# Optimization experiments

Measured on AMD Instinct MI355X. Metric: run time of the kernel, lower is better.

The kernel has to match this reference:

```python
import jax, jax.numpy as jnp
import numpy as np

N = 32                      # rotation matrix size (n x n)
INPUT_DIM = 512
HIDDEN = 1024
BATCH = 16384
NUM_ANGLES = N * (N - 1) // 2   # 496

# Givens plane indices in the same order as the original double loop:
# i = 0..n-2, j = i+1..n-1 (row-major upper triangle)
_I_IDX, _J_IDX = np.triu_indices(N, k=1)


def setup_inputs() -> dict:
    key = jax.random.key(0)
    k0, k1, k2 = jax.random.split(key, 3)
    x = jax.random.normal(k0, (BATCH, INPUT_DIM), dtype=jnp.float32)
    # nn.Linear weights: fc (hidden, input_dim), fc2 (num_angles, hidden)
    W1 = jax.random.normal(k1, (HIDDEN, INPUT_DIM), dtype=jnp.float32) / np.sqrt(INPUT_DIM)
    b1 = jnp.zeros((HIDDEN,), dtype=jnp.float32)
    W2 = jax.random.normal(k2, (NUM_ANGLES, HIDDEN), dtype=jnp.float32) / np.sqrt(HIDDEN)
    b2 = jnpups = jnp.zeros((NUM_ANGLES,), dtype=jnp.float32)
    return {"x": x, "W1": W1, "b1": b1, "W2": W2, "b2": b2}


def reference(x, W1, b1, W2, b2):
    """Faithful forward: MLP -> angles -> sequential Givens-rotation product.

    Right-multiplying R by the Givens matrix G(i, j, theta) only mixes
    columns i and j of R, so each loop iteration is a 2-column update
    instead of a full [B, n, n] bmm. Same math as the original.
    """
    B = x.shape[0]
    h = jax.nn.relu(x @ W1.T + b1)                 # [B, HIDDEN]
    angles = jnp.mod(h @ W2.T + b2, 2.0 * jnp.pi)  # [B, NUM_ANGLES]
    c_all = jnp.cos(angles).T                      # [A, B]
    s_all = jnp.sin(angles).T                      # [A, B]

    R0 = jnp.tile(jnp.eye(N, dtype=x.dtype), (B, 1, 1))  # [B, n, n]
    i_idx = jnp.asarray(_I_IDX)
    j_idx = jnp.asarray(_J_IDX)

    def step(R, inp):
        i, j, c, s = inp                # scalars i, j; c, s: [B]
        col_i = R[:, :, i]              # [B, n]
        col_j = R[:, :, j]              # [B, n]
        new_i = col_i * c[:, None] + col_j * s[:, None]
        new_j = -col_i * s[:, None] + col_j * c[:, None]
        R = R.at[:, :, i].set(new_i)
        R = R.at[:, :, j].set(new_j)
        return R, None

    R, _ = jax.lax.scan(step, R0, (i_idx, j_idx, c_all, s_all))
    return R
```

## Files before the change

### kernel.cpp

```cpp
#include <hip/hip_runtime.h>
#include <math.h>
#include <utility>

#define BATCH 16384
#define INPUT_DIM 512
#define HIDDEN 1024
#define NROT 32
#define NANG 496

typedef _Float16 half8 __attribute__((ext_vector_type(8)));
typedef _Float16 half4 __attribute__((ext_vector_type(4)));
typedef float    f32x4 __attribute__((ext_vector_type(4)));

#define NX8  (BATCH * INPUT_DIM / 8)
#define NW18 (HIDDEN * INPUT_DIM / 8)
#define NW28 (512 * HIDDEN / 8)

__global__ __launch_bounds__(256) void prep_f16(
    const float* __restrict__ x, const float* __restrict__ W1,
    const float* __restrict__ W2, _Float16* __restrict__ x16,
    _Float16* __restrict__ W116, _Float16* __restrict__ W216)
{
    const int i = blockIdx.x * 256 + threadIdx.x;
    const float* src; _Float16* dst; int j; bool zero = false;
    if (i < NX8)              { j = i;               src = x;  dst = x16;  }
    else if (i < NX8 + NW18)  { j = i - NX8;         src = W1; dst = W116; }
    else if (i < NX8 + NW18 + NW28) {
        j = i - NX8 - NW18;   src = W2; dst = W216;
        zero = (j * 8 >= NANG * HIDDEN);
    } else return;

    half8 h;
    if (zero) {
        #pragma unroll
        for (int q = 0; q < 8; ++q) h[q] = (_Float16)0.f;
    } else {
        const float4* s = (const float4*)src + (size_t)j * 2;
        const float4 a = s[0], b = s[1];
        h[0]=(_Float16)a.x; h[1]=(_Float16)a.y; h[2]=(_Float16)a.z; h[3]=(_Float16)a.w;
        h[4]=(_Float16)b.x; h[5]=(_Float16)b.y; h[6]=(_Float16)b.z; h[7]=(_Float16)b.w;
    }
    *(half8*)(dst + (size_t)j * 8) = h;
}

__device__ __forceinline__ void gld16(const void* g, void* l) {
    __builtin_amdgcn_global_load_lds(
        (const __attribute__((address_space(1))) void*)g,
        (__attribute__((address_space(3))) void*)l, 16, 0, 0);
}

template<int EPI>
__global__ __launch_bounds__(256) void gemm_nt_f16(
    const _Float16* __restrict__ A, const _Float16* __restrict__ B,
    const float* __restrict__ bias, float* __restrict__ Cf,
    _Float16* __restrict__ Ch, int M, int K, int Nout, int GX)
{
    constexpr int BK = 32;
    __shared__ _Float16 sA[2][128 * BK];
    __shared__ _Float16 sB[2][128 * BK];

    const int g  = blockIdx.x;
    const int my = (g & 7) + (((g >> 3) / GX) << 3);
    const int mx = (g >> 3) % GX;
    const int m0 = my * 128;
    const int n0 = mx * 128;

    const int tid  = threadIdx.x;
    const int lane = tid & 63;
    const int wid  = tid >> 6;

    const int srow = lane >> 2;
    const int schk = (lane & 3) ^ (srow & 3);
    const _Float16* gA0 = A + (size_t)(m0 + wid * 32 + srow) * K + schk * 8;
    const _Float16* gA1 = gA0 + (size_t)16 * K;
    const _Float16* gB0 = B + (size_t)(n0 + wid * 32 + srow) * K + schk * 8;
    const _Float16* gB1 = gB0 + (size_t)16 * K;

    auto stage = [&](int kt, int buf) {
        const size_t ko = (size_t)kt * BK;
        gld16(gA0 + ko, &sA[buf][wid * 1024]);
        gld16(gA1 + ko, &sA[buf][wid * 1024 + 512]);
        gld16(gB0 + ko, &sB[buf][wid * 1024]);
        gld16(gB1 + ko, &sB[buf][wid * 1024 + 512]);
    };

    const int wr = wid >> 1, wc = wid & 1;
    const int fr = lane & 15, fq = lane >> 4;
    const int swR   = ((fq ^ (fr & 3)) << 3);
    const int aBase = (wr * 64 + fr) * BK + swR;
    const int bBase = (wc * 64 + fr) * BK + swR;

    f32x4 acc[4][4];
    #pragma unroll
    for (int i = 0; i < 4; ++i)
        #pragma unroll
        for (int j = 0; j < 4; ++j) acc[i][j] = (f32x4)(0.f);

    const int NT = K / BK;
    stage(0, 0);
    __syncthreads();
    int cur = 0;

    for (int kt = 0; kt < NT; ++kt) {
        if (kt + 1 < NT) stage(kt + 1, cur ^ 1);

        half8 a_[4], b_[4];
        #pragma unroll
        for (int f = 0; f < 4; ++f) {
            a_[f] = *(const half8*)&sA[cur][aBase + f * 16 * BK];
            b_[f] = *(const half8*)&sB[cur][bBase + f * 16 * BK];
        }
        #pragma unroll
        for (int fm = 0; fm < 4; ++fm)
            #pragma unroll
            for (int fn = 0; fn < 4; ++fn)
                acc[fm][fn] = __builtin_amdgcn_mfma_f32_16x16x32_f16(
                    a_[fm], b_[fn], acc[fm][fn], 0, 0, 0);

        __syncthreads();
        cur ^= 1;
    }

    if (EPI == 0) {
        #pragma unroll
        for (int fn = 0; fn < 4; ++fn) {
            const int col = n0 + wc * 64 + fn * 16 + fr;
            const float bv = bias[col];
            #pragma unroll
            for (int fm = 0; fm < 4; ++fm) {
                const int row0 = m0 + wr * 64 + fm * 16 + fq * 4;
                #pragma unroll
                for (int r = 0; r < 4; ++r)
                    Ch[(size_t)(row0 + r) * Nout + col] =
                        (_Float16)fmaxf(acc[fm][fn][r] + bv, 0.f);
            }
        }
    } else {
        #pragma unroll
        for (int fn = 0; fn < 4; ++fn) {
            const int col = n0 + wc * 64 + fn * 16 + fr;
            if (col < Nout) {
                const float bv = bias[col];
                #pragma unroll
                for (int fm = 0; fm < 4; ++fm) {
                    const int row0 = m0 + wr * 64 + fm * 16 + fq * 4;
                    #pragma unroll
                    for (int r = 0; r < 4; ++r)
                        Cf[(size_t)(row0 + r) * Nout + col] = acc[fm][fn][r] + bv;
                }
            }
        }
    }
}

struct IJTbl { unsigned char i[NANG]; unsigned char j[NANG]; };
constexpr IJTbl make_ij_tbl() {
    IJTbl t{};
    int k = 0;
    for (int i = 0; i < NROT - 1; ++i)
        for (int j = i + 1; j < NROT; ++j) { t.i[k] = (unsigned char)i; t.j[k] = (unsigned char)j; ++k; }
    return t;
}
constexpr IJTbl IJT = make_ij_tbl();

#define CS_STRIDE 1000
#define SLOT_H    1040
#define EVEN_H    4224
#define ODD_H     8448
#define PCM_H     0
#define RF32      2112
#define R_STRIDE  1032

template<int M>
__device__ __forceinline__ void rot_fwd(const f32x4 q, float (&v)[NROT]) {
    {
        constexpr int k = 2 * M;
        constexpr int i = IJT.i[k], j = IJT.j[k];
        const float vi = v[i], vj = v[j];
        v[i] = fmaf(q[0], vi,  q[1] * vj);
        v[j] = fmaf(q[0], vj, -q[1] * vi);
    }
    {
        constexpr int k = 2 * M + 1;
        constexpr int i = IJT.i[k], j = IJT.j[k];
        const float vi = v[i], vj = v[j];
        v[i] = fmaf(q[2], vi,  q[3] * vj);
        v[j] = fmaf(q[2], vj, -q[3] * vi);
    }
}

template<int M>
__device__ __forceinline__ void rot_rev(const f32x4 q, float (&v)[NROT]) {
    {
        constexpr int k = 2 * M + 1;
        constexpr int i = IJT.i[k], j = IJT.j[k];
        const float vi = v[i], vj = v[j];
        v[i] = fmaf(q[2], vi, -q[3] * vj);
        v[j] = fmaf(q[2], vj,  q[3] * vi);
    }
    {
        constexpr int k = 2 * M;
        constexpr int i = IJT.i[k], j = IJT.j[k];
        const float vi = v[i], vj = v[j];
        v[i] = fmaf(q[0], vi, -q[1] * vj);
        v[j] = fmaf(q[0], vj,  q[1] * vi);
    }
}

template<int W, int T>
__device__ __forceinline__ void chain_step(const float* __restrict__ lcs,
                                           float (&v)[NROT]) {
    if constexpr ((W & 1) == 0) {
        constexpr int fi = 62 * W + T;
        const f32x4 q = *(const f32x4*)(lcs + fi * 4);
        rot_fwd<fi>(q, v);
    } else {
        constexpr int fi = 62 * W + (61 - T);
        const f32x4 q = *(const f32x4*)(lcs + fi * 4);
        rot_rev<fi>(q, v);
    }
}

template<int W, size_t... Ts>
__device__ __forceinline__ void chain_runW(const float* __restrict__ lcs,
                                           float (&v)[NROT],
                                           std::index_sequence<Ts...>) {
    (chain_step<W, (int)Ts>(lcs, v), ...);
}

template<int W>
__device__ __forceinline__ void chain_and_store(const float* __restrict__ lcs,
                                                _Float16* __restrict__ lh,
                                                int half, int r) {
    float v[NROT];
    #pragma unroll
    for (int c = 0; c < NROT; ++c) v[c] = (c == r) ? 1.f : 0.f;
    chain_runW<W>(lcs, v, std::make_index_sequence<62>{});

    constexpr int REG = ((W & 1) == 0) ? EVEN_H : ODD_H;
    const int base = REG + (half * 2 + (W >> 1)) * SLOT_H;
    #pragma unroll
    for (int kq = 0; kq < 4; ++kq) {
        half8 hv;
        #pragma unroll
        for (int j = 0; j < 8; ++j) hv[j] = (_Float16)v[kq * 8 + j];
        *(half8*)&lh[base + r * 32 + ((kq ^ (r & 3)) << 3)] = hv;
    }
}

__global__ __launch_bounds__(256) void rotate_kernel(
    const float* __restrict__ theta, float* __restrict__ out)
{
    __shared__ float smem[6304];
    _Float16* lh = (_Float16*)smem;

    const int tid  = threadIdx.x;
    const int wid  = tid >> 6;
    const int lane = tid & 63;
    const int half = (tid >> 5) & 1;
    const int r    = tid & 31;
    const int fr = lane & 15, fq = lane >> 4;
    const size_t b0 = (size_t)blockIdx.x * 2;

    if (tid < 248) {
        const int b   = tid >= 124;
        const int idx = tid - b * 124;
        const f32x4 th = *(const f32x4*)(theta + b0 * NANG + (size_t)(b * NANG) + idx * 4);
        f32x4 p0, p1;
        float s, c;
        __sincosf(th[0], &s, &c); p0[0] = c; p0[1] = s;
        __sincosf(th[1], &s, &c); p0[2] = c; p0[3] = s;
        __sincosf(th[2], &s, &c); p1[0] = c; p1[1] = s;
        __sincosf(th[3], &s, &c); p1[2] = c; p1[3] = s;
        const int base = b * CS_STRIDE + idx * 8;
        *(f32x4*)&smem[base]     = p0;
        *(f32x4*)&smem[base + 4] = p1;
    }
    __syncthreads();

    const float* lcs = smem + half * CS_STRIDE;
    if      (wid == 0) chain_and_store<0>(lcs, lh, half, r);
    else if (wid == 1) chain_and_store<1>(lcs, lh, half, r);
    else if (wid == 2) chain_and_store<2>(lcs, lh, half, r);
    else               chain_and_store<3>(lcs, lh, half, r);
    __syncthreads();

    {
        const int ba = wid >> 1, pi = wid & 1;
        const int Eb = EVEN_H + (ba * 2 + pi) * SLOT_H;
        const int Ob = ODD_H  + (ba * 2 + pi) * SLOT_H;
        const int Asrc = (pi == 0) ? Ob : Eb;
        const int Bsrc = (pi == 0) ? Eb : Ob;
        const int swz = (fq ^ (fr & 3)) << 3;
        half8 a[2], b[2];
        #pragma unroll
        for (int mi = 0; mi < 2; ++mi) {
            a[mi] = *(const half8*)&lh[Asrc + (mi * 16 + fr) * 32 + swz];
            b[mi] = *(const half8*)&lh[Bsrc + (mi * 16 + fr) * 32 + swz];
        }
        const int Pb = PCM_H + (ba * 2 + pi) * SLOT_H;
        #pragma unroll
        for (int mi = 0; mi < 2; ++mi)
            #pragma unroll
            for (int ni = 0; ni < 2; ++ni) {
                const f32x4 d = __builtin_amdgcn_mfma_f32_16x16x32_f16(
                    a[mi], b[ni], (f32x4)(0.f), 0, 0, 0);
                half4 hv;
                #pragma unroll
                for (int q = 0; q < 4; ++q) hv[q] = (_Float16)d[q];
                const int col  = ni * 16 + fr;
                const int rowb = (mi * 16 + fq * 4) ^ ((col & 3) << 3);
                *(half4*)&lh[Pb + col * 32 + rowb] = hv;
            }
    }
    __syncthreads();

    {
        const int ba = wid >> 1, mi = wid & 1;
        const int Ab = PCM_H + (ba * 2 + 1) * SLOT_H;
        const int Bb = PCM_H + (ba * 2 + 0) * SLOT_H;
        const int swz = (fq ^ (fr & 3)) << 3;
        const half8 a = *(const half8*)&lh[Ab + (mi * 16 + fr) * 32 + swz];
        #pragma unroll
        for (int ni = 0; ni < 2; ++ni) {
            const half8 b = *(const half8*)&lh[Bb + (ni * 16 + fr) * 32 + swz];
            const f32x4 d = __builtin_amdgcn_mfma_f32_16x16x32_f16(
                a, b, (f32x4)(0.f), 0, 0, 0);
            const int row  = ni * 16 + fr;
            const int colq = mi * 4 + fq;
            *(f32x4*)&smem[RF32 + ba * R_STRIDE + row * 32 + ((colq ^ (row & 7)) << 2)] = d;
        }
    }
    __syncthreads();

    #pragma unroll
    for (int s = 0; s < 2; ++s) {
        const int idx = s * 256 + tid;
        const int ba  = idx >> 8;
        const int f4i = idx & 255;
        const int row = f4i >> 3;
        const int cc  = f4i & 7;
        const f32x4 val =
            *(const f32x4*)&smem[RF32 + ba * R_STRIDE + row * 32 + ((cc ^ (row & 7)) << 2)];
        *(f32x4*)(out + (b0 + ba) * 1024 + (size_t)f4i * 4) = val;
    }
}

extern "C" void kernel_launch(void* const* d_in, const int* in_sizes, int n_in,
                              void* d_out, int out_size, void* d_ws, size_t ws_size,
                              hipStream_t stream)
{
    const float* x  = (const float*)d_in[0];
    const float* W1 = (const float*)d_in[1];
    const float* b1 = (const float*)d_in[2];
    const float* W2 = (const float*)d_in[3];
    const float* b2 = (const float*)d_in[4];
    float* out = (float*)d_out;

    _Float16* h16  = (_Float16*)d_out;
    _Float16* x16  = h16  + (size_t)BATCH * HIDDEN;
    _Float16* W116 = x16  + (size_t)BATCH * INPUT_DIM;
    _Float16* W216 = W116 + (size_t)HIDDEN * INPUT_DIM;
    float*    th   = (float*)d_ws;

    prep_f16<<<dim3((NX8 + NW18 + NW28) / 256), 256, 0, stream>>>(
        x, W1, W2, x16, W116, W216);

    gemm_nt_f16<0><<<dim3(8 * 128), 256, 0, stream>>>(
        x16, W116, b1, nullptr, h16, BATCH, INPUT_DIM, HIDDEN, 8);

    gemm_nt_f16<1><<<dim3(4 * 128), 256, 0, stream>>>(
        h16, W216, b2, th, nullptr, BATCH, HIDDEN, NANG, 4);

    rotate_kernel<<<dim3(BATCH / 2), 256, 0, stream>>>(th, out);
}
```

Measured before the change: 112.0 us.

## Pack two rotation rows per lane with v_pk_fma and process four batches per block

```diff
diff --git a/kernel.cpp b/kernel.cpp
--- a/kernel.cpp
+++ b/kernel.cpp
@@ -11,6 +11,7 @@
 typedef _Float16 half8 __attribute__((ext_vector_type(8)));
 typedef _Float16 half4 __attribute__((ext_vector_type(4)));
 typedef float    f32x4 __attribute__((ext_vector_type(4)));
+typedef float    f32x2 __attribute__((ext_vector_type(2)));
 
 #define NX8  (BATCH * INPUT_DIM / 8)
 #define NW18 (HIDDEN * INPUT_DIM / 8)
@@ -165,65 +166,56 @@
 
 #define CS_STRIDE 1000
 #define SLOT_H    1040
-#define EVEN_H    4224
-#define ODD_H     8448
 #define PCM_H     0
-#define RF32      2112
+#define EVEN_H    8320
+#define ODD_H     16640
+#define RF32      4160
 #define R_STRIDE  1032
 
-template<int M>
-__device__ __forceinline__ void rot_fwd(const f32x4 q, float (&v)[NROT]) {
-    {
-        constexpr int k = 2 * M;
-        constexpr int i = IJT.i[k], j = IJT.j[k];
-        const float vi = v[i], vj = v[j];
-        v[i] = fmaf(q[0], vi,  q[1] * vj);
-        v[j] = fmaf(q[0], vj, -q[1] * vi);
-    }
-    {
-        constexpr int k = 2 * M + 1;
-        constexpr int i = IJT.i[k], j = IJT.j[k];
-        const float vi = v[i], vj = v[j];
-        v[i] = fmaf(q[2], vi,  q[3] * vj);
-        v[j] = fmaf(q[2], vj, -q[3] * vi);
-    }
-}
-
-template<int M>
-__device__ __forceinline__ void rot_rev(const f32x4 q, float (&v)[NROT]) {
-    {
-        constexpr int k = 2 * M + 1;
-        constexpr int i = IJT.i[k], j = IJT.j[k];
-        const float vi = v[i], vj = v[j];
-        v[i] = fmaf(q[2], vi, -q[3] * vj);
-        v[j] = fmaf(q[2], vj,  q[3] * vi);
-    }
-    {
-        constexpr int k = 2 * M;
-        constexpr int i = IJT.i[k], j = IJT.j[k];
-        const float vi = v[i], vj = v[j];
-        v[i] = fmaf(q[0], vi, -q[1] * vj);
-        v[j] = fmaf(q[0], vj,  q[1] * vi);
-    }
+__device__ __forceinline__ f32x2 lo2(const f32x4 q) { return __builtin_shufflevector(q, q, 0, 1); }
+__device__ __forceinline__ f32x2 hi2(const f32x4 q) { return __builtin_shufflevector(q, q, 2, 3); }
+
+template<int K, bool REV>
+__device__ __forceinline__ void rot1pk(const f32x2 p, f32x2 (&v)[NROT]) {
+    constexpr int i = IJT.i[K], j = IJT.j[K];
+    f32x2 t0, t1, ni, nj;
+    asm("v_pk_mul_f32 %0, %1, %2 op_sel:[1,0] op_sel_hi:[1,1]"
+        : "=v"(t0) : "v"(p), "v"(v[j]));
+    asm("v_pk_mul_f32 %0, %1, %2 op_sel:[1,0] op_sel_hi:[1,1]"
+        : "=v"(t1) : "v"(p), "v"(v[i]));
+    if constexpr (!REV) {
+        asm("v_pk_fma_f32 %0, %1, %2, %3 op_sel:[0,0,0] op_sel_hi:[0,1,1]"
+            : "=v"(ni) : "v"(p), "v"(v[i]), "v"(t0));
+        asm("v_pk_fma_f32 %0, %1, %2, %3 op_sel:[0,0,0] op_sel_hi:[0,1,1] neg_lo:[0,0,1] neg_hi:[0,0,1]"
+            : "=v"(nj) : "v"(p), "v"(v[j]), "v"(t1));
+    } else {
+        asm("v_pk_fma_f32 %0, %1, %2, %3 op_sel:[0,0,0] op_sel_hi:[0,1,1] neg_lo:[0,0,1] neg_hi:[0,0,1]"
+            : "=v"(ni) : "v"(p), "v"(v[i]), "v"(t0));
+        asm("v_pk_fma_f32 %0, %1, %2, %3 op_sel:[0,0,0] op_sel_hi:[0,1,1]"
+            : "=v"(nj) : "v"(p), "v"(v[j]), "v"(t1));
+    }
+    v[i] = ni; v[j] = nj;
 }
 
 template<int W, int T>
 __device__ __forceinline__ void chain_step(const float* __restrict__ lcs,
-                                           float (&v)[NROT]) {
+                                           f32x2 (&v)[NROT]) {
     if constexpr ((W & 1) == 0) {
         constexpr int fi = 62 * W + T;
         const f32x4 q = *(const f32x4*)(lcs + fi * 4);
-        rot_fwd<fi>(q, v);
+        rot1pk<2 * fi,     false>(lo2(q), v);
+        rot1pk<2 * fi + 1, false>(hi2(q), v);
     } else {
         constexpr int fi = 62 * W + (61 - T);
         const f32x4 q = *(const f32x4*)(lcs + fi * 4);
-        rot_rev<fi>(q, v);
+        rot1pk<2 * fi + 1, true>(hi2(q), v);
+        rot1pk<2 * fi,     true>(lo2(q), v);
     }
 }
 
 template<int W, size_t... Ts>
 __device__ __forceinline__ void chain_runW(const float* __restrict__ lcs,
-                                           float (&v)[NROT],
+                                           f32x2 (&v)[NROT],
                                            std::index_sequence<Ts...>) {
     (chain_step<W, (int)Ts>(lcs, v), ...);
 }
@@ -231,110 +223,130 @@
 template<int W>
 __device__ __forceinline__ void chain_and_store(const float* __restrict__ lcs,
                                                 _Float16* __restrict__ lh,
-                                                int half, int r) {
-    float v[NROT];
-    #pragma unroll
-    for (int c = 0; c < NROT; ++c) v[c] = (c == r) ? 1.f : 0.f;
+                                                int b, int rp) {
+    f32x2 v[NROT];
+    #pragma unroll
+    for (int c = 0; c < NROT; ++c) {
+        f32x2 iv;
+        iv[0] = (c == rp)      ? 1.f : 0.f;
+        iv[1] = (c == rp + 16) ? 1.f : 0.f;
+        v[c] = iv;
+    }
     chain_runW<W>(lcs, v, std::make_index_sequence<62>{});
 
     constexpr int REG = ((W & 1) == 0) ? EVEN_H : ODD_H;
-    const int base = REG + (half * 2 + (W >> 1)) * SLOT_H;
+    const int base = REG + (b * 2 + (W >> 1)) * SLOT_H;
     #pragma unroll
     for (int kq = 0; kq < 4; ++kq) {
-        half8 hv;
-        #pragma unroll
-        for (int j = 0; j < 8; ++j) hv[j] = (_Float16)v[kq * 8 + j];
-        *(half8*)&lh[base + r * 32 + ((kq ^ (r & 3)) << 3)] = hv;
+        half8 h0, h1;
+        #pragma unroll
+        for (int j = 0; j < 8; ++j) {
+            h0[j] = (_Float16)v[kq * 8 + j][0];
+            h1[j] = (_Float16)v[kq * 8 + j][1];
+        }
+        const int sw = (kq ^ (rp & 3)) << 3;
+        *(half8*)&lh[base +  rp       * 32 + sw] = h0;
+        *(half8*)&lh[base + (rp + 16) * 32 + sw] = h1;
     }
 }
 
 __global__ __launch_bounds__(256) void rotate_kernel(
     const float* __restrict__ theta, float* __restrict__ out)
 {
-    __shared__ float smem[6304];
+    __shared__ float smem[12480];
     _Float16* lh = (_Float16*)smem;
 
     const int tid  = threadIdx.x;
     const int wid  = tid >> 6;
     const int lane = tid & 63;
-    const int half = (tid >> 5) & 1;
-    const int r    = tid & 31;
+    const int lb   = lane >> 4;
+    const int rp   = lane & 15;
     const int fr = lane & 15, fq = lane >> 4;
-    const size_t b0 = (size_t)blockIdx.x * 2;
-
-    if (tid < 248) {
-        const int b   = tid >= 124;
-        const int idx = tid - b * 124;
-        const f32x4 th = *(const f32x4*)(theta + b0 * NANG + (size_t)(b * NANG) + idx * 4);
-        f32x4 p0, p1;
-        float s, c;
-        __sincosf(th[0], &s, &c); p0[0] = c; p0[1] = s;
-        __sincosf(th[1], &s, &c); p0[2] = c; p0[3] = s;
-        __sincosf(th[2], &s, &c); p1[0] = c; p1[1] = s;
-        __sincosf(th[3], &s, &c); p1[2] = c; p1[3] = s;
-        const int base = b * CS_STRIDE + idx * 8;
-        *(f32x4*)&smem[base]     = p0;
-        *(f32x4*)&smem[base + 4] = p1;
-    }
-    __syncthreads();
-
-    const float* lcs = smem + half * CS_STRIDE;
-    if      (wid == 0) chain_and_store<0>(lcs, lh, half, r);
-    else if (wid == 1) chain_and_store<1>(lcs, lh, half, r);
-    else if (wid == 2) chain_and_store<2>(lcs, lh, half, r);
-    else               chain_and_store<3>(lcs, lh, half, r);
+    const size_t b0 = (size_t)blockIdx.x * 4;
+
+    #pragma unroll
+    for (int it = 0; it < 2; ++it) {
+        const int t = it * 256 + tid;
+        if (t < 496) {
+            const int b   = t / 124;
+            const int idx = t - b * 124;
+            const f32x4 th = *(const f32x4*)(theta + (b0 + b) * NANG + idx * 4);
+            f32x4 p0, p1;
+            float s, c;
+            __sincosf(th[0], &s, &c); p0[0] = c; p0[1] = s;
+            __sincosf(th[1], &s, &c); p0[2] = c; p0[3] = s;
+            __sincosf(th[2], &s, &c); p1[0] = c; p1[1] = s;
+            __sincosf(th[3], &s, &c); p1[2] = c; p1[3] = s;
+            const int base = b * CS_STRIDE + idx * 8;
+            *(f32x4*)&smem[base]     = p0;
+            *(f32x4*)&smem[base + 4] = p1;
+        }
+    }
+    __syncthreads();
+
+    const float* lcs = smem + lb * CS_STRIDE;
+    if      (wid == 0) chain_and_store<0>(lcs, lh, lb, rp);
+    else if (wid == 1) chain_and_store<1>(lcs, lh, lb, rp);
+    else if (wid == 2) chain_and_store<2>(lcs, lh, lb, rp);
+    else               chain_and_store<3>(lcs, lh, lb, rp);
     __syncthreads();
 
     {
-        const int ba = wid >> 1, pi = wid & 1;
-        const int Eb = EVEN_H + (ba * 2 + pi) * SLOT_H;
-        const int Ob = ODD_H  + (ba * 2 + pi) * SLOT_H;
-        const int Asrc = (pi == 0) ? Ob : Eb;
-        const int Bsrc = (pi == 0) ? Eb : Ob;
+        const int ba = wid;
         const int swz = (fq ^ (fr & 3)) << 3;
-        half8 a[2], b[2];
-        #pragma unroll
-        for (int mi = 0; mi < 2; ++mi) {
-            a[mi] = *(const half8*)&lh[Asrc + (mi * 16 + fr) * 32 + swz];
-            b[mi] = *(const half8*)&lh[Bsrc + (mi * 16 + fr) * 32 + swz];
-        }
-        const int Pb = PCM_H + (ba * 2 + pi) * SLOT_H;
-        #pragma unroll
-        for (int mi = 0; mi < 2; ++mi)
-            #pragma unroll
-            for (int ni = 0; ni < 2; ++ni) {
-                const f32x4 d = __builtin_amdgcn_mfma_f32_16x16x32_f16(
-                    a[mi], b[ni], (f32x4)(0.f), 0, 0, 0);
-                half4 hv;
+        #pragma unroll
+        for (int pi = 0; pi < 2; ++pi) {
+            const int Eb = EVEN_H + (ba * 2 + pi) * SLOT_H;
+            const int Ob = ODD_H  + (ba * 2 + pi) * SLOT_H;
+            const int Asrc = (pi == 0) ? Ob : Eb;
+            const int Bsrc = (pi == 0) ? Eb : Ob;
+            half8 a[2], b[2];
+            #pragma unroll
+            for (int mi = 0; mi < 2; ++mi) {
+                a[mi] = *(const half8*)&lh[Asrc + (mi * 16 + fr) * 32 + swz];
+                b[mi] = *(const half8*)&lh[Bsrc + (mi * 16 + fr) * 32 + swz];
+            }
+            const int Pb = PCM_H + (ba * 2 + pi) * SLOT_H;
+            #pragma unroll
+            for (int mi = 0; mi < 2; ++mi)
                 #pragma unroll
-                for (int q = 0; q < 4; ++q) hv[q] = (_Float16)d[q];
-                const int col  = ni * 16 + fr;
-                const int rowb = (mi * 16 + fq * 4) ^ ((col & 3) << 3);
-                *(half4*)&lh[Pb + col * 32 + rowb] = hv;
-            }
+                for (int ni = 0; ni < 2; ++ni) {
+                    const f32x4 d = __builtin_amdgcn_mfma_f32_16x16x32_f16(
+                        a[mi], b[ni], (f32x4)(0.f), 0, 0, 0);
+                    half4 hv;
+                    #pragma unroll
+                    for (int q = 0; q < 4; ++q) hv[q] = (_Float16)d[q];
+                    const int col  = ni * 16 + fr;
+                    const int rowb = (mi * 16 + fq * 4) ^ ((col & 3) << 3);
+                    *(half4*)&lh[Pb + col * 32 + rowb] = hv;
+                }
+        }
     }
     __syncthreads();
 
     {
-        const int ba = wid >> 1, mi = wid & 1;
+        const int ba = wid;
         const int Ab = PCM_H + (ba * 2 + 1) * SLOT_H;
         const int Bb = PCM_H + (ba * 2 + 0) * SLOT_H;
         const int swz = (fq ^ (fr & 3)) << 3;
-        const half8 a = *(const half8*)&lh[Ab + (mi * 16 + fr) * 32 + swz];
-        #pragma unroll
-        for (int ni = 0; ni < 2; ++ni) {
-            const half8 b = *(const half8*)&lh[Bb + (ni * 16 + fr) * 32 + swz];
-            const f32x4 d = __builtin_amdgcn_mfma_f32_16x16x32_f16(
-                a, b, (f32x4)(0.f), 0, 0, 0);
-            const int row  = ni * 16 + fr;
-            const int colq = mi * 4 + fq;
-            *(f32x4*)&smem[RF32 + ba * R_STRIDE + row * 32 + ((colq ^ (row & 7)) << 2)] = d;
-        }
-    }
-    __syncthreads();
-
-    #pragma unroll
-    for (int s = 0; s < 2; ++s) {
+        #pragma unroll
+        for (int mi = 0; mi < 2; ++mi) {
+            const half8 a = *(const half8*)&lh[Ab + (mi * 16 + fr) * 32 + swz];
+            #pragma unroll
+            for (int ni = 0; ni < 2; ++ni) {
+                const half8 b = *(const half8*)&lh[Bb + (ni * 16 + fr) * 32 + swz];
+                const f32x4 d = __builtin_amdgcn_mfma_f32_16x16x32_f16(
+                    a, b, (f32x4)(0.f), 0, 0, 0);
+                const int row  = ni * 16 + fr;
+                const int colq = mi * 4 + fq;
+                *(f32x4*)&smem[RF32 + ba * R_STRIDE + row * 32 + ((colq ^ (row & 7)) << 2)] = d;
+            }
+        }
+    }
+    __syncthreads();
+
+    #pragma unroll
+    for (int s = 0; s < 4; ++s) {
         const int idx = s * 256 + tid;
         const int ba  = idx >> 8;
         const int f4i = idx & 255;
@@ -372,5 +384,5 @@
     gemm_nt_f16<1><<<dim3(4 * 128), 256, 0, stream>>>(
         h16, W216, b2, th, nullptr, BATCH, HIDDEN, NANG, 4);
 
-    rotate_kernel<<<dim3(BATCH / 2), 256, 0, stream>>>(th, out);
-}
+    rotate_kernel<<<dim3(BATCH / 4), 256, 0, stream>>>(th, out);
+}
```

Result: faster. 104.8 us (-6.5%).
